# Optimization experiments

Measured on AMD Instinct MI355X. Metric: run time of the kernel, lower is better.

## Reference

```python
import jax, jax.numpy as jnp
import numpy as np
import math

T, C = 8192, 1024

def setup_inputs() -> dict:
    key = jax.random.key(0)
    ks = jax.random.split(key, 10)
    s = 1.0 / math.sqrt(C)
    return {
        "x": jax.random.normal(ks[0], (T, C), dtype=jnp.float32),
        "Wq": jax.random.normal(ks[1], (C, C), dtype=jnp.float32) * s,
        "bq": jax.random.normal(ks[2], (C,), dtype=jnp.float32) * s,
        "Wk": jax.random.normal(ks[3], (C, C), dtype=jnp.float32) * s,
        "bk": jax.random.normal(ks[4], (C,), dtype=jnp.float32) * s,
        "Wv": jax.random.normal(ks[5], (C, C), dtype=jnp.float32) * s,
        "bv": jax.random.normal(ks[6], (C,), dtype=jnp.float32) * s,
        "Wp": jax.random.normal(ks[7], (C, C), dtype=jnp.float32) * s,
        "bp": jax.random.normal(ks[8], (C,), dtype=jnp.float32) * s,
    }

def reference(x, Wq, bq, Wk, bk, Wv, bv, Wp, bp):
    # Single-head causal self-attention over an unbatched (T, C) sequence.
    t, c = x.shape
    q = x @ Wq.T + bq          # (T, C)
    k = x @ Wk.T + bk          # (T, C)
    v = x @ Wv.T + bv          # (T, C)
    att = (q @ k.T) / math.sqrt(c)                      # (T, T)
    causal = jnp.tril(jnp.ones((t, t), dtype=bool))
    att = jnp.where(causal, att, -jnp.inf)
    att = jax.nn.softmax(att, axis=-1)
    y = att @ v                                         # (T, C)
    y = y @ Wp.T + bp
    return y
```

## Files before the change

kernel.cpp:

```cpp
#include <hip/hip_runtime.h>
#include <hip/hip_bf16.h>

typedef __bf16 bf16x8 __attribute__((ext_vector_type(8)));
typedef float f32x4 __attribute__((ext_vector_type(4)));

static constexpr int Tn = 8192;
static constexpr int Cn = 1024;

#define DEVI __device__ __forceinline__

DEVI float bf2f(ushort u) { union { uint i; float f; } c; c.i = ((uint)u) << 16; return c.f; }
DEVI ushort f2bf(float f) {
  uint x = __builtin_bit_cast(uint, f);
  x += 0x7fffu + ((x >> 16) & 1u);
  return (ushort)(x >> 16);
}

typedef const __attribute__((address_space(1))) void glb_v;
typedef __attribute__((address_space(3))) void lds_v;

#define BAR()   __builtin_amdgcn_s_barrier()
#define SCH0()  __builtin_amdgcn_sched_barrier(0)
#define PRIO1() __builtin_amdgcn_s_setprio(1)
#define PRIO0() __builtin_amdgcn_s_setprio(0)

__global__ __launch_bounds__(256) void cast_all(
    const float* __restrict__ x, const float* __restrict__ wq, const float* __restrict__ wk,
    const float* __restrict__ wv, const float* __restrict__ wp,
    const float* __restrict__ bq, const float* __restrict__ bk, const float* __restrict__ bv,
    ushort* __restrict__ xb, ushort* __restrict__ wqkv, ushort* __restrict__ wpb,
    float* __restrict__ bqkv, float* __restrict__ lsum)
{
  const long long NX = (long long)Tn * Cn;
  const long long NW = (long long)Cn * Cn;
  if (blockIdx.x == 12291) {
    float4 z; z.x = z.y = z.z = z.w = 0.f;
#pragma unroll
    for (int j = 0; j < 8; ++j) ((float4*)lsum)[threadIdx.x * 8 + j] = z;
    return;
  }
  if (blockIdx.x >= 12288) {
    int id = ((blockIdx.x - 12288) * 256 + threadIdx.x) * 4;
#pragma unroll
    for (int e = 0; e < 4; ++e) {
      int j = id + e;
      if (j < 3 * Cn) bqkv[j] = j < Cn ? bq[j] : (j < 2 * Cn ? bk[j - Cn] : bv[j - 2 * Cn]);
    }
    return;
  }
  long long i = ((long long)blockIdx.x * 256 + threadIdx.x) * 4;
  const float* src; ushort* dst; long long off;
  if (i < NX) { src = x; dst = xb; off = i; }
  else {
    long long r = i - NX; int seg = (int)(r >> 20); off = r & (NW - 1);
    if (seg < 3) { src = seg == 0 ? wq : seg == 1 ? wk : wv; dst = wqkv + (size_t)seg * NW; }
    else         { src = wp; dst = wpb; }
  }
  float4 v = *reinterpret_cast<const float4*>(src + off);
  ushort4 o; o.x = f2bf(v.x); o.y = f2bf(v.y); o.z = f2bf(v.z); o.w = f2bf(v.w);
  *reinterpret_cast<ushort4*>(dst + off) = o;
}

__global__ __launch_bounds__(256) void zero_acc(float4* __restrict__ p)
{
  const int i = (blockIdx.x * 256 + threadIdx.x) * 4;
  float4 z; z.x = z.y = z.z = z.w = 0.f;
#pragma unroll
  for (int j = 0; j < 4; ++j) p[i + j] = z;
}

__global__ __launch_bounds__(256) void ydiv(const float* __restrict__ Yacc,
                                            const float* __restrict__ lsum,
                                            ushort* __restrict__ Yb)
{
  const int i = (blockIdx.x * 256 + threadIdx.x) * 8;
  const int row = i >> 10;
  const float inv = 1.0f / lsum[row];
  float4 a = *reinterpret_cast<const float4*>(Yacc + i);
  float4 b = *reinterpret_cast<const float4*>(Yacc + i + 4);
  union { uint4 v; ushort u[8]; } pk;
  pk.u[0] = f2bf(a.x * inv); pk.u[1] = f2bf(a.y * inv);
  pk.u[2] = f2bf(a.z * inv); pk.u[3] = f2bf(a.w * inv);
  pk.u[4] = f2bf(b.x * inv); pk.u[5] = f2bf(b.y * inv);
  pk.u[6] = f2bf(b.z * inv); pk.u[7] = f2bf(b.w * inv);
  *reinterpret_cast<uint4*>(Yb + i) = pk.v;
}

template<bool OUT_BF16, bool HAS_BIAS, bool QKT, bool PVM, bool SPLIT3>
__global__ __launch_bounds__(256, 2)
void gemm_rp(const ushort* __restrict__ A, const ushort* __restrict__ Bt,
             const float* __restrict__ bias, void* __restrict__ outp,
             float* __restrict__ lsum,
             int K, int lda, int ldb, int ldc, float scale)
{
  __shared__ __align__(16) ushort sm[32768];

  const int tid = threadIdx.x, lane = tid & 63, wid = tid >> 6;
  const int wm = wid >> 1, wn = wid & 1;
  const int ln15 = lane & 15, lsec = lane >> 4;

  int bx, by;
  if (QKT) {
    by = blockIdx.x; bx = blockIdx.y;
    if (by < bx) return;
  } else {
    bx = blockIdx.x; by = blockIdx.y;
  }
  const int rowA0 = by * 128, col0 = bx * 128;

  int t0 = 0, NT = K >> 6;
  if (PVM) {
    int ktot = (by + 1) * 2;
    if (ktot > (K >> 6)) ktot = K >> 6;
    const int nz = (int)gridDim.z, bz = (int)blockIdx.z;
    const int q = ktot / nz, r = ktot % nz;
    const int len = q + (bz < r ? 1 : 0);
    if (len == 0) return;
    t0 = bz < r ? bz * (q + 1) : r * (q + 1) + (bz - r) * q;
    NT = t0 + len;
  }

  const uint smb = (uint)(uintptr_t)&sm[0];

  auto stage = [&](int t, int b) {
    const int tt = t < NT ? t : NT - 1;
    const size_t k0 = (size_t)(tt << 6);
#pragma unroll
    for (int i = 0; i < 4; ++i) {
      int s = tid + i * 256; int row = s >> 3; int kcs = (s & 7) ^ (row & 7);
      const ushort* g = A + (size_t)(rowA0 + row) * (size_t)lda + k0 + kcs * 8;
      __builtin_amdgcn_global_load_lds((glb_v*)g, (lds_v*)(&sm[b * 16384 + s * 8]), 16, 0, 0);
    }
#pragma unroll
    for (int i = 0; i < 4; ++i) {
      int s = tid + i * 256; int row = s >> 3; int kcs = (s & 7) ^ (row & 7);
      const ushort* g = Bt + (size_t)(col0 + row) * (size_t)ldb + k0 + kcs * 8;
      __builtin_amdgcn_global_load_lds((glb_v*)g, (lds_v*)(&sm[b * 16384 + 8192 + s * 8]), 16, 0, 0);
    }
  };

  uint offA[2][4], offB[2][4];
#pragma unroll
  for (int ks = 0; ks < 2; ++ks) {
    int kc = ks * 4 + lsec;
#pragma unroll
    for (int mi = 0; mi < 4; ++mi) {
      int r = wm * 64 + mi * 16 + ln15;
      offA[ks][mi] = (uint)((r * 64 + (kc ^ (r & 7)) * 8) * 2);
    }
#pragma unroll
    for (int ni = 0; ni < 4; ++ni) {
      int c = wn * 64 + ni * 16 + ln15;
      offB[ks][ni] = (uint)(16384 + (c * 64 + (kc ^ (c & 7)) * 8) * 2);
    }
  }

  bf16x8 f0A[4], f0B[4], f1A[4], f1B[4];
  f32x4 acc[4][4] = {};

#define DSR(d, a) asm volatile("ds_read_b128 %0, %1" : "=v"(d) : "v"(a))
#define MMAC(FA, FB) { _Pragma("unroll") for (int mi = 0; mi < 4; ++mi) \
    _Pragma("unroll") for (int ni = 0; ni < 4; ++ni) \
      acc[mi][ni] = __builtin_amdgcn_mfma_f32_16x16x32_bf16(FA[mi], FB[ni], acc[mi][ni], 0, 0, 0); }

  stage(t0, 0); stage(t0 + 1, 1);
  asm volatile("s_waitcnt vmcnt(8)" ::: "memory");
  BAR();
  SCH0();
#pragma unroll
  for (int mi = 0; mi < 4; ++mi) DSR(f0A[mi], smb + offA[0][mi]);
#pragma unroll
  for (int ni = 0; ni < 4; ++ni) DSR(f0B[ni], smb + offB[0][ni]);
  SCH0();

  uint boff = 0;
  const int len = NT - t0;
  for (int it = 0; it < len; ++it, boff ^= 32768u) {
#pragma unroll
    for (int mi = 0; mi < 4; ++mi) DSR(f1A[mi], smb + boff + offA[1][mi]);
#pragma unroll
    for (int ni = 0; ni < 4; ++ni) DSR(f1B[ni], smb + boff + offB[1][ni]);
    SCH0();
    asm volatile("s_waitcnt lgkmcnt(8)" ::: "memory");
    SCH0();
    PRIO1(); MMAC(f0A, f0B); PRIO0();
    SCH0();
    asm volatile("s_waitcnt lgkmcnt(0)" ::: "memory");
    BAR();
    stage(t0 + it + 2, it & 1);
    SCH0();
    asm volatile("s_waitcnt vmcnt(8)" ::: "memory");
    BAR();
    SCH0();
    const uint bo1 = boff ^ 32768u;
#pragma unroll
    for (int mi = 0; mi < 4; ++mi) DSR(f0A[mi], smb + bo1 + offA[0][mi]);
#pragma unroll
    for (int ni = 0; ni < 4; ++ni) DSR(f0B[ni], smb + bo1 + offB[0][ni]);
    SCH0();
    PRIO1(); MMAC(f1A, f1B); PRIO0();
    SCH0();
  }
  asm volatile("s_waitcnt vmcnt(0) lgkmcnt(0)" ::: "memory");
#undef DSR
#undef MMAC

  if constexpr (QKT) {
#pragma unroll
    for (int mi = 0; mi < 4; ++mi) {
#pragma unroll
      for (int j = 0; j < 4; ++j) {
        const int row = rowA0 + wm * 64 + mi * 16 + lsec * 4 + j;
        float rs = 0.f;
        ushort pb[4];
#pragma unroll
        for (int ni = 0; ni < 4; ++ni) {
          const int col = col0 + wn * 64 + ni * 16 + ln15;
          float p = 0.f;
          if (col <= row) p = __expf(acc[mi][ni][j] * scale);
          pb[ni] = f2bf(p);
          rs += bf2f(pb[ni]);
        }
#pragma unroll
        for (int o = 1; o < 16; o <<= 1) rs += __shfl_xor(rs, o);
        if (ln15 == 0) atomicAdd(&lsum[row], rs);
#pragma unroll
        for (int ni = 0; ni < 4; ++ni) {
          const int col = col0 + wn * 64 + ni * 16 + ln15;
          ((ushort*)outp)[(size_t)row * (size_t)ldc + col] = pb[ni];
        }
      }
    }
  } else if constexpr (PVM) {
    float* Yacc = (float*)outp;
#pragma unroll
    for (int mi = 0; mi < 4; ++mi) {
#pragma unroll
      for (int j = 0; j < 4; ++j) {
        const int row = rowA0 + wm * 64 + mi * 16 + lsec * 4 + j;
#pragma unroll
        for (int ni = 0; ni < 4; ++ni) {
          const int col = col0 + wn * 64 + ni * 16 + ln15;
          atomicAdd(&Yacc[(size_t)row * (size_t)ldc + col], acc[mi][ni][j]);
        }
      }
    }
  } else {
#pragma unroll
    for (int mi = 0; mi < 4; ++mi) {
#pragma unroll
      for (int j = 0; j < 4; ++j) {
        const int row = rowA0 + wm * 64 + mi * 16 + lsec * 4 + j;
#pragma unroll
        for (int ni = 0; ni < 4; ++ni) {
          const int colg = col0 + wn * 64 + ni * 16 + ln15;
          float val = acc[mi][ni][j] * scale;
          if constexpr (HAS_BIAS) val += bias[colg];
          int col = colg; size_t segoff = 0;
          if constexpr (SPLIT3) { int seg = colg >> 10; col = colg & 1023; segoff = (size_t)seg * (size_t)Tn * Cn; }
          if constexpr (OUT_BF16) ((ushort*)outp)[segoff + (size_t)row * (size_t)ldc + col] = f2bf(val);
          else                    ((float*)outp)[segoff + (size_t)row * (size_t)ldc + col] = val;
        }
      }
    }
  }
}

__global__ __launch_bounds__(256) void transpose64(const ushort* __restrict__ in,
                                                   ushort* __restrict__ out,
                                                   int ldin, int ldout)
{
  __shared__ ushort tile[64][65];
  const int c0 = blockIdx.x * 64, r0 = blockIdx.y * 64;
  const int t = threadIdx.x;
#pragma unroll
  for (int i = t; i < 512; i += 256) {
    int r = i >> 3, kc = i & 7;
    uint4 v = *reinterpret_cast<const uint4*>(in + (size_t)(r0 + r) * ldin + c0 + kc * 8);
    const ushort* u = reinterpret_cast<const ushort*>(&v);
#pragma unroll
    for (int j = 0; j < 8; ++j) tile[r][kc * 8 + j] = u[j];
  }
  __syncthreads();
#pragma unroll
  for (int i = t; i < 512; i += 256) {
    int c = i >> 3, rc = i & 7;
    union { uint4 v; ushort u[8]; } pk;
#pragma unroll
    for (int j = 0; j < 8; ++j) pk.u[j] = tile[rc * 8 + j][c];
    *reinterpret_cast<uint4*>(out + (size_t)(c0 + c) * ldout + r0 + rc * 8) = pk.v;
  }
}

extern "C" void kernel_launch(void* const* d_in, const int* in_sizes, int n_in,
                              void* d_out, int out_size, void* d_ws, size_t ws_size,
                              hipStream_t stream)
{
  (void)in_sizes; (void)n_in; (void)out_size; (void)ws_size;
  const float* x  = (const float*)d_in[0];
  const float* Wq = (const float*)d_in[1];
  const float* bq = (const float*)d_in[2];
  const float* Wk = (const float*)d_in[3];
  const float* bk = (const float*)d_in[4];
  const float* Wv = (const float*)d_in[5];
  const float* bv = (const float*)d_in[6];
  const float* Wp = (const float*)d_in[7];
  const float* bp = (const float*)d_in[8];

  char* w = (char*)d_ws;
  const size_t TC = (size_t)Tn * Cn * 2, CC = (size_t)Cn * Cn * 2;
  ushort* xb   = (ushort*)w; w += TC;
  ushort* Wqkv = (ushort*)w; w += 3 * CC;
  ushort* wpb  = (ushort*)w; w += CC;
  float*  bqkv = (float*)w;  w += 16384;
  float*  lsum = (float*)w;  w += 32768;
  ushort* Qb   = (ushort*)w; w += TC;
  ushort* Kb   = (ushort*)w; w += TC;
  ushort* Vb   = (ushort*)w; w += TC;
  ushort* Vt   = (ushort*)w; w += TC;
  ushort* Yb   = (ushort*)w; w += TC;
  ushort* S    = (ushort*)w; w += (size_t)Tn * Tn * 2;
  float*  Yacc = (float*)Qb;

  cast_all<<<12292, 256, 0, stream>>>(x, Wq, Wk, Wv, Wp, bq, bk, bv,
                                      xb, Wqkv, wpb, bqkv, lsum);

  gemm_rp<true, true, false, false, true><<<dim3(24, 64), 256, 0, stream>>>(
      xb, Wqkv, bqkv, Qb, nullptr, Cn, Cn, Cn, Cn, 1.0f);

  transpose64<<<dim3(Cn / 64, Tn / 64), 256, 0, stream>>>(Vb, Vt, Cn, Tn);

  gemm_rp<true, false, true, false, false><<<dim3(64, 64), 256, 0, stream>>>(
      Qb, Kb, nullptr, S, lsum, Cn, Cn, Cn, Tn, 0.03125f);

  zero_acc<<<2048, 256, 0, stream>>>((float4*)Yacc);

  gemm_rp<false, false, false, true, false><<<dim3(8, 64, 4), 256, 0, stream>>>(
      S, Vt, nullptr, Yacc, nullptr, Tn, Tn, Tn, Cn, 1.0f);

  ydiv<<<4096, 256, 0, stream>>>(Yacc, lsum, Yb);

  gemm_rp<false, true, false, false, false><<<dim3(8, 64), 256, 0, stream>>>(
      Yb, wpb, bp, d_out, nullptr, Cn, Cn, Cn, Cn, 1.0f);
}
```

Baseline: 368.0 us.

## Replace atomic split-K PV with two-way bf16 partials and compact causal QK grid

The QK^T launch now uses a compact 1D grid of only the lower-triangular tiles, ordered in 8-row groups, so no blocks are launched only to exit early. The PV GEMM splits K into exactly two halves per row tile, writes bf16 partials into two buffers instead of fp32 atomics, and launches heaviest rows first. The zero-init kernel is dropped, and ydiv now sums the two bf16 partials before normalising. This removes atomic traffic and a launch, but adds bf16 rounding on the partial sums and may leave load imbalance with only two splits.

```diff
diff --git a/kernel.cpp b/kernel.cpp
--- a/kernel.cpp
+++ b/kernel.cpp
@@ -61,28 +61,21 @@
   *reinterpret_cast<ushort4*>(dst + off) = o;
 }
 
-__global__ __launch_bounds__(256) void zero_acc(float4* __restrict__ p)
-{
-  const int i = (blockIdx.x * 256 + threadIdx.x) * 4;
-  float4 z; z.x = z.y = z.z = z.w = 0.f;
-#pragma unroll
-  for (int j = 0; j < 4; ++j) p[i + j] = z;
-}
-
-__global__ __launch_bounds__(256) void ydiv(const float* __restrict__ Yacc,
+__global__ __launch_bounds__(256) void ydiv(const ushort* __restrict__ P0,
+                                            const ushort* __restrict__ P1,
                                             const float* __restrict__ lsum,
                                             ushort* __restrict__ Yb)
 {
   const int i = (blockIdx.x * 256 + threadIdx.x) * 8;
   const int row = i >> 10;
   const float inv = 1.0f / lsum[row];
-  float4 a = *reinterpret_cast<const float4*>(Yacc + i);
-  float4 b = *reinterpret_cast<const float4*>(Yacc + i + 4);
+  uint4 a = *reinterpret_cast<const uint4*>(P0 + i);
+  uint4 b = *reinterpret_cast<const uint4*>(P1 + i);
+  const ushort* ua = reinterpret_cast<const ushort*>(&a);
+  const ushort* ub = reinterpret_cast<const ushort*>(&b);
   union { uint4 v; ushort u[8]; } pk;
-  pk.u[0] = f2bf(a.x * inv); pk.u[1] = f2bf(a.y * inv);
-  pk.u[2] = f2bf(a.z * inv); pk.u[3] = f2bf(a.w * inv);
-  pk.u[4] = f2bf(b.x * inv); pk.u[5] = f2bf(b.y * inv);
-  pk.u[6] = f2bf(b.z * inv); pk.u[7] = f2bf(b.w * inv);
+#pragma unroll
+  for (int e = 0; e < 8; ++e) pk.u[e] = f2bf((bf2f(ua[e]) + bf2f(ub[e])) * inv);
   *reinterpret_cast<uint4*>(Yb + i) = pk.v;
 }
 
@@ -90,7 +83,7 @@
 __global__ __launch_bounds__(256, 2)
 void gemm_rp(const ushort* __restrict__ A, const ushort* __restrict__ Bt,
              const float* __restrict__ bias, void* __restrict__ outp,
-             float* __restrict__ lsum,
+             void* __restrict__ outp2, float* __restrict__ lsum,
              int K, int lda, int ldb, int ldc, float scale)
 {
   __shared__ __align__(16) ushort sm[32768];
@@ -99,25 +92,32 @@
   const int wm = wid >> 1, wn = wid & 1;
   const int ln15 = lane & 15, lsec = lane >> 4;
 
-  int bx, by;
-  if (QKT) {
-    by = blockIdx.x; bx = blockIdx.y;
-    if (by < bx) return;
+  int bx, by, zsel = 0;
+  if constexpr (QKT) {
+    int id = blockIdx.x, g = 0;
+    for (;;) { int sz = 36 + 8 * (56 - 8 * g); if (id < sz || g == 7) break; id -= sz; ++g; }
+    int r, c;
+    if (id < 36) {
+      int d = 0;
+      while ((d + 1) * (d + 2) / 2 <= id) ++d;
+      c = id - d * (d + 1) / 2; r = d;
+    } else {
+      int q = id - 36; r = 8 + (q >> 3); c = q & 7;
+    }
+    by = 8 * g + r; bx = 8 * g + c;
+  } else if constexpr (PVM) {
+    by = 63 - ((int)blockIdx.x >> 4);
+    bx = ((int)blockIdx.x >> 1) & 7;
+    zsel = (int)blockIdx.x & 1;
   } else {
     bx = blockIdx.x; by = blockIdx.y;
   }
   const int rowA0 = by * 128, col0 = bx * 128;
 
   int t0 = 0, NT = K >> 6;
-  if (PVM) {
-    int ktot = (by + 1) * 2;
-    if (ktot > (K >> 6)) ktot = K >> 6;
-    const int nz = (int)gridDim.z, bz = (int)blockIdx.z;
-    const int q = ktot / nz, r = ktot % nz;
-    const int len = q + (bz < r ? 1 : 0);
-    if (len == 0) return;
-    t0 = bz < r ? bz * (q + 1) : r * (q + 1) + (bz - r) * q;
-    NT = t0 + len;
+  if constexpr (PVM) {
+    const int half = by + 1;
+    t0 = zsel * half; NT = t0 + half;
   }
 
   const uint smb = (uint)(uintptr_t)&sm[0];
@@ -232,7 +232,7 @@
       }
     }
   } else if constexpr (PVM) {
-    float* Yacc = (float*)outp;
+    ushort* dst = (ushort*)(zsel ? outp2 : outp);
 #pragma unroll
     for (int mi = 0; mi < 4; ++mi) {
 #pragma unroll
@@ -241,7 +241,7 @@
 #pragma unroll
         for (int ni = 0; ni < 4; ++ni) {
           const int col = col0 + wn * 64 + ni * 16 + ln15;
-          atomicAdd(&Yacc[(size_t)row * (size_t)ldc + col], acc[mi][ni][j]);
+          dst[(size_t)row * (size_t)ldc + col] = f2bf(acc[mi][ni][j]);
         }
       }
     }
@@ -320,26 +320,23 @@
   ushort* Vt   = (ushort*)w; w += TC;
   ushort* Yb   = (ushort*)w; w += TC;
   ushort* S    = (ushort*)w; w += (size_t)Tn * Tn * 2;
-  float*  Yacc = (float*)Qb;
 
   cast_all<<<12292, 256, 0, stream>>>(x, Wq, Wk, Wv, Wp, bq, bk, bv,
                                       xb, Wqkv, wpb, bqkv, lsum);
 
   gemm_rp<true, true, false, false, true><<<dim3(24, 64), 256, 0, stream>>>(
-      xb, Wqkv, bqkv, Qb, nullptr, Cn, Cn, Cn, Cn, 1.0f);
+      xb, Wqkv, bqkv, Qb, nullptr, nullptr, Cn, Cn, Cn, Cn, 1.0f);
 
   transpose64<<<dim3(Cn / 64, Tn / 64), 256, 0, stream>>>(Vb, Vt, Cn, Tn);
 
-  gemm_rp<true, false, true, false, false><<<dim3(64, 64), 256, 0, stream>>>(
-      Qb, Kb, nullptr, S, lsum, Cn, Cn, Cn, Tn, 0.03125f);
-
-  zero_acc<<<2048, 256, 0, stream>>>((float4*)Yacc);
-
-  gemm_rp<false, false, false, true, false><<<dim3(8, 64, 4), 256, 0, stream>>>(
-      S, Vt, nullptr, Yacc, nullptr, Tn, Tn, Tn, Cn, 1.0f);
-
-  ydiv<<<4096, 256, 0, stream>>>(Yacc, lsum, Yb);
+  gemm_rp<true, false, true, false, false><<<dim3(2080), 256, 0, stream>>>(
+      Qb, Kb, nullptr, S, nullptr, lsum, Cn, Cn, Cn, Tn, 0.03125f);
+
+  gemm_rp<true, false, false, true, false><<<dim3(1024), 256, 0, stream>>>(
+      S, Vt, nullptr, Qb, Vb, nullptr, Tn, Tn, Tn, Cn, 1.0f);
+
+  ydiv<<<4096, 256, 0, stream>>>(Qb, Vb, lsum, Yb);
 
   gemm_rp<false, true, false, false, false><<<dim3(8, 64), 256, 0, stream>>>(
-      Yb, wpb, bp, d_out, nullptr, Cn, Cn, Cn, Cn, 1.0f);
-}
+      Yb, wpb, bp, d_out, nullptr, nullptr, Cn, Cn, Cn, Cn, 1.0f);
+}
```

Measured after the change: 298.1 us. 1.23x faster.
